# Kernel tuning notes

Measured on AMD Instinct MI355X. Metric: run time of the kernel, lower is better.

## Reference

```python
import jax, jax.numpy as jnp
from jax import lax
import numpy as np

# Dims
B_, CIN, COUT, T = 2, 64, 128, 8192
K, NM, N, DCONV, EXP = 5, 2, 16, 4, 2   # kernel, n_mamba, d_state, d_conv, expand
DI = EXP * COUT                          # d_inner = 256
DTR = (COUT + 15) // 16                  # dt_rank = 8
M = NM * 2                               # mamba instances (fwd+bwd per block)


def setup_inputs() -> dict:
    key = jax.random.key(0)
    ks = jax.random.split(key, 8)
    r = lambda k, s, sc=0.02: (jax.random.normal(k, s) * sc).astype(jnp.float32)
    return {
        "x": jax.random.normal(ks[0], (B_, CIN, T), dtype=jnp.float32),
        "conv_w": r(ks[1], (COUT, CIN, K), 0.05),
        "conv_b": jnp.zeros((COUT,), jnp.float32),
        "gn_g": jnp.ones((COUT,), jnp.float32),
        "gn_b": jnp.zeros((COUT,), jnp.float32),
        "prelu_a": jnp.full((1,), 0.25, jnp.float32),
        "ln_g": jnp.ones((NM, COUT), jnp.float32),
        "ln_b": jnp.zeros((NM, COUT), jnp.float32),
        "W_in": r(ks[2], (M, 2 * DI, COUT)),
        "conv1d_w": r(ks[3], (M, DI, 1, DCONV), 0.1),
        "conv1d_b": jnp.zeros((M, DI), jnp.float32),
        "W_xproj": r(ks[4], (M, DTR + 2 * N, DI)),
        "W_dt": r(ks[5], (M, DI, DTR), 0.1),
        "b_dt": jnp.full((M, DI), -4.0, jnp.float32),
        "A_log": jnp.broadcast_to(jnp.log(jnp.arange(1, N + 1, dtype=jnp.float32)), (M, DI, N)).copy(),
        "D_param": jnp.ones((M, DI), jnp.float32),
        "W_out": r(ks[6], (M, COUT, DI)),
    }


def _silu(x):
    return x * jax.nn.sigmoid(x)


def _layernorm(x, g, b, eps=1e-5):
    mu = x.mean(-1, keepdims=True)
    v = ((x - mu) ** 2).mean(-1, keepdims=True)
    return (x - mu) * lax.rsqrt(v + eps) * g + b


def _mamba(h, Wi, cw, cb, Wx, Wd, bd, Alog, Dp, Wo):
    # h: [B, L, d_model] -> [B, L, d_model]. Standard Mamba (S6) block.
    Bb, L, _ = h.shape
    xz = jnp.einsum('bld,ed->ble', h, Wi)               # [B,L,2*DI]
    xp, z = jnp.split(xz, 2, axis=-1)
    xc = jnp.transpose(xp, (0, 2, 1))                   # [B,DI,L]
    xc = lax.conv_general_dilated(xc, cw, (1,), [(DCONV - 1, 0)],
                                  feature_group_count=DI,
                                  dimension_numbers=('NCH', 'OIH', 'NCH')) + cb[None, :, None]
    u = _silu(jnp.transpose(xc, (0, 2, 1)))             # [B,L,DI]
    xdbl = jnp.einsum('bld,ed->ble', u, Wx)             # [B,L,DTR+2N]
    dt, Bm, Cm = jnp.split(xdbl, [DTR, DTR + N], axis=-1)
    delta = jax.nn.softplus(jnp.einsum('blr,dr->bld', dt, Wd) + bd)  # [B,L,DI]
    A = -jnp.exp(Alog)                                  # [DI,N]
    dA = jnp.exp(delta[..., None] * A)                  # [B,L,DI,N]
    dBu = (delta * u)[..., None] * Bm[:, :, None, :]    # [B,L,DI,N]

    def step(hc, inp):
        a, b, c = inp
        hc = a * hc + b                                  # [B,DI,N]
        return hc, jnp.einsum('bdn,bn->bd', hc, c)

    h0 = jnp.zeros((Bb, DI, N), dtype=h.dtype)
    _, ys = lax.scan(step, h0, (jnp.moveaxis(dA, 1, 0), jnp.moveaxis(dBu, 1, 0), jnp.moveaxis(Cm, 1, 0)))
    y = jnp.moveaxis(ys, 0, 1) + u * Dp                 # [B,L,DI]
    y = y * _silu(z)
    return jnp.einsum('ble,de->bld', y, Wo)


def reference(x, conv_w, conv_b, gn_g, gn_b, prelu_a, ln_g, ln_b, W_in,
              conv1d_w, conv1d_b, W_xproj, W_dt, b_dt, A_log, D_param, W_out):
    # Conv1d stride 2, padding K//2: [B,CIN,T] -> [B,COUT,T//2]
    h = lax.conv_general_dilated(x, conv_w, (2,), [(K // 2, K // 2)],
                                 dimension_numbers=('NCH', 'OIH', 'NCH')) + conv_b[None, :, None]
    # GroupNorm(1, COUT): normalize jointly over (C, T)
    mu = h.mean((1, 2), keepdims=True)
    v = ((h - mu) ** 2).mean((1, 2), keepdims=True)
    h = (h - mu) * lax.rsqrt(v + 1e-5) * gn_g[None, :, None] + gn_b[None, :, None]
    h = jnp.where(h >= 0, h, prelu_a[0] * h)            # PReLU (shared scalar)
    h = jnp.transpose(h, (0, 2, 1))                     # [B, L, C]
    for i in range(NM):
        hn = _layernorm(h, ln_g[i], ln_b[i])
        f, bw = 2 * i, 2 * i + 1
        yf = _mamba(hn, W_in[f], conv1d_w[f], conv1d_b[f], W_xproj[f], W_dt[f], b_dt[f], A_log[f], D_param[f], W_out[f])
        hb = jnp.flip(hn, axis=1)
        yb = jnp.flip(_mamba(hb, W_in[bw], conv1d_w[bw], conv1d_b[bw], W_xproj[bw], W_dt[bw], b_dt[bw], A_log[bw], D_param[bw], W_out[bw]), axis=1)
        h = h + yf + yb                                  # bidirectional residual
    return jnp.transpose(h, (0, 2, 1))                   # [B, COUT, T//2]
```

## Files before the change

### kernel.cpp

```cpp
#include <hip/hip_runtime.h>
#include <hip/hip_bf16.h>
#include <math.h>

constexpr int B2   = 2;
constexpr int CIN  = 64;
constexpr int COUT = 128;
constexpr int T    = 8192;
constexpr int L    = 4096;
constexpr int DI   = 256;
constexpr int NST  = 16;
constexpr int DTR  = 8;
constexpr int Q    = 32;
constexpr int NC   = 128;
constexpr int TOK  = B2 * L;

typedef __attribute__((ext_vector_type(8))) short bf16x8s;
typedef __attribute__((ext_vector_type(4))) float f32x4;

__device__ __forceinline__ float sigmoidf_(float x) { return 1.f / (1.f + __expf(-x)); }
__device__ __forceinline__ unsigned short f2bf(float f) {
    unsigned int u = __float_as_uint(f);
    unsigned int r = (u + 0x7FFFu + ((u >> 16) & 1u)) >> 16;
    return (unsigned short)r;
}
__device__ __forceinline__ float bf2f(unsigned short s) {
    return __uint_as_float((unsigned int)s << 16);
}

__global__ __launch_bounds__(256) void prep_all_kernel(
    const float* __restrict__ W_in, const float* __restrict__ W_out,
    const float* __restrict__ cw,
    unsigned short* __restrict__ Winb, unsigned short* __restrict__ Woutb,
    unsigned short* __restrict__ Wrb, float* __restrict__ stats) {
    int idx = blockIdx.x * 256 + threadIdx.x;
    if (blockIdx.x == 0 && threadIdx.x < 4) stats[threadIdx.x] = 0.f;
    if (idx < 262144) {
        Winb[idx] = f2bf(W_in[idx]);
    } else if (idx < 393216) {
        int i = idx - 262144; Woutb[i] = f2bf(W_out[i]);
    } else if (idx < 434176) {
        int i = idx - 393216;
        int co = i / 320, r = i % 320;
        int kp = r >> 6, ci = r & 63;
        Wrb[i] = f2bf(cw[co * 320 + ci * 5 + kp]);
    }
}

__global__ __launch_bounds__(256) void xpose_kernel(
    const float* __restrict__ x, unsigned short* __restrict__ xTb) {
    __shared__ float tile[64][65];
    int b = blockIdx.y, tb = blockIdx.x * 64, tid = threadIdx.x;
    #pragma unroll
    for (int i = 0; i < 16; ++i) {
        int idx = i * 256 + tid; int ci = idx >> 6, tt = idx & 63;
        tile[ci][tt] = x[((size_t)b * CIN + ci) * T + tb + tt];
    }
    __syncthreads();
    #pragma unroll
    for (int i = 0; i < 16; ++i) {
        int idx = i * 256 + tid; int tt = idx >> 6, ci = idx & 63;
        xTb[((size_t)b * T + tb + tt) * 64 + ci] = f2bf(tile[ci][tt]);
    }
}

__global__ __launch_bounds__(256) void conv_mfma_kernel(
    const unsigned short* __restrict__ xTb, const unsigned short* __restrict__ Wrb,
    const float* __restrict__ cb, float* __restrict__ h, float* __restrict__ stats) {
    const int tid = threadIdx.x;
    const int w = tid >> 6, lane = tid & 63, q = lane >> 4, c = lane & 15;
    const int t0g = blockIdx.x * 64;
    const int t0  = t0g + w * 16;
    const int ct0 = blockIdx.y * 64;
    const int b   = t0g >> 12;
    const int l   = (t0 + c) & (L - 1);
    f32x4 acc[4] = {};
    for (int kc = 0; kc < 320; kc += 32) {
        int kp  = kc >> 6;
        int ci0 = (kc & 63) + q * 8;
        int p = 2 * l + kp - 2;
        bf16x8s a = {};
        if (p >= 0 && p < T)
            a = *(const bf16x8s*)&xTb[((size_t)b * T + p) * 64 + ci0];
        #pragma unroll
        for (int i = 0; i < 4; ++i) {
            bf16x8s bb = *(const bf16x8s*)&Wrb[(size_t)(ct0 + i * 16 + c) * 320 + kc + q * 8];
            acc[i] = __builtin_amdgcn_mfma_f32_16x16x32_bf16(a, bb, acc[i], 0, 0, 0);
        }
    }
    float s = 0.f, ss = 0.f;
    #pragma unroll
    for (int i = 0; i < 4; ++i) {
        int cout = ct0 + i * 16 + c;
        float bias = cb[cout];
        #pragma unroll
        for (int r = 0; r < 4; ++r) {
            int tok = t0 + q * 4 + r;
            float v = acc[i][r] + bias;
            h[(size_t)tok * COUT + cout] = v;
            s += v; ss += v * v;
        }
    }
    #pragma unroll
    for (int off = 32; off; off >>= 1) {
        s  += __shfl_down(s,  off, 64);
        ss += __shfl_down(ss, off, 64);
    }
    if (lane == 0) {
        atomicAdd(&stats[b * 2 + 0], s);
        atomicAdd(&stats[b * 2 + 1], ss);
    }
}

__global__ __launch_bounds__(256) void gn_ln_kernel(
    float* __restrict__ h, const float* __restrict__ gn_g,
    const float* __restrict__ gn_b, const float* __restrict__ prelu_a,
    const float* __restrict__ stats, unsigned short* __restrict__ hnb,
    const float* __restrict__ lng, const float* __restrict__ lnb) {
    int wave = threadIdx.x >> 6, lane = threadIdx.x & 63;
    int t = blockIdx.x * 4 + wave;
    int b = t >> 12;
    const float n = (float)(L * COUT);
    float mu   = stats[b * 2 + 0] / n;
    float var  = stats[b * 2 + 1] / n - mu * mu;
    float rstd = rsqrtf(var + 1e-5f);
    float a = prelu_a[0];
    float* row = h + (size_t)t * COUT;
    float2 v  = *(const float2*)&row[lane * 2];
    float2 g  = *(const float2*)&gn_g[lane * 2];
    float2 bb = *(const float2*)&gn_b[lane * 2];
    v.x = (v.x - mu) * rstd * g.x + bb.x; v.x = v.x >= 0.f ? v.x : a * v.x;
    v.y = (v.y - mu) * rstd * g.y + bb.y; v.y = v.y >= 0.f ? v.y : a * v.y;
    *(float2*)&row[lane * 2] = v;
    float s = v.x + v.y, ss = v.x * v.x + v.y * v.y;
    #pragma unroll
    for (int off = 32; off; off >>= 1) {
        s  += __shfl_xor(s,  off, 64);
        ss += __shfl_xor(ss, off, 64);
    }
    float mu2 = s * (1.f / 128.f);
    float var2 = ss * (1.f / 128.f) - mu2 * mu2;
    float rstd2 = rsqrtf(var2 + 1e-5f);
    float2 gg = *(const float2*)&lng[lane * 2];
    float2 lb = *(const float2*)&lnb[lane * 2];
    ushort2 o;
    o.x = f2bf((v.x - mu2) * rstd2 * gg.x + lb.x);
    o.y = f2bf((v.y - mu2) * rstd2 * gg.y + lb.y);
    *(ushort2*)&hnb[(size_t)t * COUT + lane * 2] = o;
}

__global__ __launch_bounds__(256) void ln_kernel(
    const float* __restrict__ h, unsigned short* __restrict__ hnb,
    const float* __restrict__ g, const float* __restrict__ bta) {
    int wave = threadIdx.x >> 6, lane = threadIdx.x & 63;
    int t = blockIdx.x * 4 + wave;
    const float* row = h + (size_t)t * COUT;
    float2 v = *(const float2*)&row[lane * 2];
    float s = v.x + v.y, ss = v.x * v.x + v.y * v.y;
    #pragma unroll
    for (int off = 32; off; off >>= 1) {
        s  += __shfl_xor(s,  off, 64);
        ss += __shfl_xor(ss, off, 64);
    }
    float mu = s * (1.f / 128.f);
    float var = ss * (1.f / 128.f) - mu * mu;
    float rstd = rsqrtf(var + 1e-5f);
    float2 gg = *(const float2*)&g[lane * 2];
    float2 bb = *(const float2*)&bta[lane * 2];
    ushort2 o;
    o.x = f2bf((v.x - mu) * rstd * gg.x + bb.x);
    o.y = f2bf((v.y - mu) * rstd * gg.y + bb.y);
    *(ushort2*)&hnb[(size_t)t * COUT + lane * 2] = o;
}

__global__ __launch_bounds__(256) void inproj_dw_kernel(
    const unsigned short* __restrict__ hnb, const unsigned short* __restrict__ Winb,
    const float* __restrict__ cw, const float* __restrict__ cbias,
    float* __restrict__ u0, float* __restrict__ u1,
    unsigned short* __restrict__ zb0, unsigned short* __restrict__ zb1, int layer) {
    __shared__ float xs[80 * 68];
    const int tid = threadIdx.x;
    const int w = tid >> 6, lane = tid & 63, q = lane >> 4, c = lane & 15;
    const int tBase = blockIdx.x * 64;
    const int nBase = blockIdx.y * 64;
    const int inst = nBase >> 9;
    const int e0 = nBase & 511;
    const int m = layer * 2 + inst;
    const unsigned short* Wb = Winb + (size_t)m * 512 * 128;

    if (e0 >= 256) {
        const int t0 = tBase + w * 16;
        f32x4 acc[4] = {};
        for (int kc = 0; kc < 128; kc += 32) {
            bf16x8s a = *(const bf16x8s*)&hnb[(size_t)(t0 + c) * 128 + kc + q * 8];
            #pragma unroll
            for (int i = 0; i < 4; ++i) {
                bf16x8s bb = *(const bf16x8s*)&Wb[(size_t)(e0 + i * 16 + c) * 128 + kc + q * 8];
                acc[i] = __builtin_amdgcn_mfma_f32_16x16x32_bf16(a, bb, acc[i], 0, 0, 0);
            }
        }
        unsigned short* zb = inst ? zb1 : zb0;
        #pragma unroll
        for (int i = 0; i < 4; ++i) {
            int eo = (e0 + i * 16 + c) & 255;
            #pragma unroll
            for (int r = 0; r < 4; ++r) {
                int tok = t0 + q * 4 + r;
                float v = acc[i][r];
                zb[(size_t)tok * DI + eo] = f2bf(v * sigmoidf_(v));
            }
        }
        return;
    }
    const int winT0 = (inst == 0) ? (tBase - 16) : tBase;
    for (int pass = 0; pass < 2; ++pass) {
        if (pass == 1 && w != 0) break;
        int slot = (pass == 0) ? (w + (inst == 0 ? 1 : 0))
                               : ((inst == 0) ? 0 : 4);
        int tokA = winT0 + slot * 16 + c;
        tokA = tokA < 0 ? 0 : (tokA > TOK - 1 ? TOK - 1 : tokA);
        f32x4 acc[4] = {};
        for (int kc = 0; kc < 128; kc += 32) {
            bf16x8s a = *(const bf16x8s*)&hnb[(size_t)tokA * 128 + kc + q * 8];
            #pragma unroll
            for (int i = 0; i < 4; ++i) {
                bf16x8s bb = *(const bf16x8s*)&Wb[(size_t)(e0 + i * 16 + c) * 128 + kc + q * 8];
                acc[i] = __builtin_amdgcn_mfma_f32_16x16x32_bf16(a, bb, acc[i], 0, 0, 0);
            }
        }
        #pragma unroll
        for (int i = 0; i < 4; ++i)
            #pragma unroll
            for (int r = 0; r < 4; ++r)
                xs[(slot * 16 + q * 4 + r) * 68 + i * 16 + c] = acc[i][r];
    }
    __syncthreads();
    const int l0base = tBase & (L - 1);
    const int ch4 = tid & 15;
    const int d0 = e0 + ch4 * 4;
    float4 w0 = *(const float4*)&cw[(size_t)(m * DI + d0 + 0) * 4];
    float4 w1 = *(const float4*)&cw[(size_t)(m * DI + d0 + 1) * 4];
    float4 w2 = *(const float4*)&cw[(size_t)(m * DI + d0 + 2) * 4];
    float4 w3 = *(const float4*)&cw[(size_t)(m * DI + d0 + 3) * 4];
    float4 bias4 = *(const float4*)&cbias[m * DI + d0];
    float* ud = inst ? u1 : u0;
    #pragma unroll
    for (int p = 0; p < 4; ++p) {
        int j = p * 16 + (tid >> 4);
        float4 acc = bias4;
        #pragma unroll
        for (int k = 0; k < 4; ++k) {
            bool valid = (inst == 0) ? (l0base + j - 3 + k >= 0)
                                     : (l0base + j + 3 - k < L);
            if (valid) {
                int wj = (inst == 0) ? (j + 13 + k) : (j + 3 - k);
                float4 v = *(const float4*)&xs[wj * 68 + ch4 * 4];
                float wk0 = ((const float*)&w0)[k], wk1 = ((const float*)&w1)[k];
                float wk2 = ((const float*)&w2)[k], wk3 = ((const float*)&w3)[k];
                acc.x = fmaf(wk0, v.x, acc.x); acc.y = fmaf(wk1, v.y, acc.y);
                acc.z = fmaf(wk2, v.z, acc.z); acc.w = fmaf(wk3, v.w, acc.w);
            }
        }
        acc.x *= sigmoidf_(acc.x); acc.y *= sigmoidf_(acc.y);
        acc.z *= sigmoidf_(acc.z); acc.w *= sigmoidf_(acc.w);
        *(float4*)&ud[(size_t)(tBase + j) * DI + d0] = acc;
    }
}

__global__ __launch_bounds__(256) void xproj_kernel(
    const float* __restrict__ u0, const float* __restrict__ u1,
    const float* __restrict__ Wx, const float* __restrict__ Wdt,
    const float* __restrict__ bdt,
    float* __restrict__ dl0, float* __restrict__ dl1,
    float* __restrict__ Bm0, float* __restrict__ Bm1,
    float* __restrict__ Cm0, float* __restrict__ Cm1, int layer) {
    __shared__ float Ws[40 * 132];
    __shared__ float As[128 * 33];
    __shared__ float xd[32 * 9];
    const int tid   = threadIdx.x;
    const int tBase = blockIdx.x * 32;
    const int inst  = blockIdx.y;
    const int m     = layer * 2 + inst;
    const float* u  = inst ? u1 : u0;
    const float* Wm = Wx + (size_t)m * 40 * 256;
    const int t  = tid & 31;
    const int eq = tid >> 5;
    float acc[5] = {};
    for (int kc = 0; kc < 256; kc += 128) {
        __syncthreads();
        #pragma unroll
        for (int i = 0; i < 5; ++i) {
            int idx = i * 256 + tid;
            int e = idx >> 5, kq = idx & 31;
            float4 w4 = *(const float4*)&Wm[(size_t)e * 256 + kc + kq * 4];
            float* dstw = &Ws[e * 132 + kq * 4];
            dstw[0] = w4.x; dstw[1] = w4.y; dstw[2] = w4.z; dstw[3] = w4.w;
        }
        #pragma unroll
        for (int i = 0; i < 4; ++i) {
            int flat = i * 256 + tid;
            int tt = flat >> 5, kq = flat & 31;
            float4 v = *(const float4*)&u[(size_t)(tBase + tt) * DI + kc + kq * 4];
            As[(kq * 4 + 0) * 33 + tt] = v.x;
            As[(kq * 4 + 1) * 33 + tt] = v.y;
            As[(kq * 4 + 2) * 33 + tt] = v.z;
            As[(kq * 4 + 3) * 33 + tt] = v.w;
        }
        __syncthreads();
        #pragma unroll 4
        for (int kk = 0; kk < 128; ++kk) {
            float a = As[kk * 33 + t];
            acc[0] = fmaf(a, Ws[(eq     ) * 132 + kk], acc[0]);
            acc[1] = fmaf(a, Ws[(eq +  8) * 132 + kk], acc[1]);
            acc[2] = fmaf(a, Ws[(eq + 16) * 132 + kk], acc[2]);
            acc[3] = fmaf(a, Ws[(eq + 24) * 132 + kk], acc[3]);
            acc[4] = fmaf(a, Ws[(eq + 32) * 132 + kk], acc[4]);
        }
    }
    {
        int tok = tBase + t;
        float* Bm = inst ? Bm1 : Bm0;
        float* Cm = inst ? Cm1 : Cm0;
        xd[t * 9 + eq] = acc[0];
        Bm[(size_t)tok * NST + eq]     = acc[1];
        Bm[(size_t)tok * NST + 8 + eq] = acc[2];
        Cm[(size_t)tok * NST + eq]     = acc[3];
        Cm[(size_t)tok * NST + 8 + eq] = acc[4];
    }
    __syncthreads();
    {
        int d = tid;
        float wr[8];
        #pragma unroll
        for (int r = 0; r < 8; ++r) wr[r] = Wdt[((size_t)m * DI + d) * DTR + r];
        float bb = bdt[m * DI + d];
        float* dl = inst ? dl1 : dl0;
        #pragma unroll 4
        for (int tt = 0; tt < 32; ++tt) {
            float a2 = bb;
            #pragma unroll
            for (int r = 0; r < 8; ++r) a2 = fmaf(xd[tt * 9 + r], wr[r], a2);
            float sp = fmaxf(a2, 0.f) + __logf(1.f + __expf(-fabsf(a2)));
            dl[(size_t)(tBase + tt) * DI + d] = sp;
        }
    }
}

__global__ __launch_bounds__(256) void scan1_kernel(
    const float* __restrict__ dl0, const float* __restrict__ dl1,
    const float* __restrict__ u0,  const float* __restrict__ u1,
    const float* __restrict__ Bm0, const float* __restrict__ Bm1,
    const float* __restrict__ A_log,
    float* __restrict__ hend, float* __restrict__ dsumb, int layer) {
    const int tid = threadIdx.x;
    const int nq = tid & 3, dlane = tid >> 2;
    const int chunk = blockIdx.x & (NC - 1), dtile = blockIdx.x >> 7;
    const int b = blockIdx.y, inst = blockIdx.z;
    const int m = layer * 2 + inst, dir = inst;
    const int d = dtile * 64 + dlane;
    const float* dl = inst ? dl1 : dl0;
    const float* u  = inst ? u1  : u0;
    const float* Bm = inst ? Bm1 : Bm0;
    float4 av = *(const float4*)&A_log[((size_t)m * DI + d) * NST + nq * 4];
    const float a0 = -expf(av.x), a1 = -expf(av.y), a2 = -expf(av.z), a3 = -expf(av.w);
    const int s0 = chunk * Q;
    const int l0 = dir ? (L - 1 - s0) : s0;
    const int stp = dir ? -1 : 1;
    long iDU = ((long)(b * L + l0)) * DI + d;
    int  iB  = ((b * L + l0) << 4) + nq * 4;
    const long sDU = (long)stp * DI;
    const int  sB  = stp * NST;
    float h0 = 0.f, h1 = 0.f, h2 = 0.f, h3 = 0.f, dsum = 0.f;
    #pragma unroll 4
    for (int t = 0; t < Q; ++t) {
        float dlt = dl[iDU], uu = u[iDU];
        float4 bm = *(const float4*)&Bm[iB];
        float du = dlt * uu;
        h0 = fmaf(__expf(dlt * a0), h0, du * bm.x);
        h1 = fmaf(__expf(dlt * a1), h1, du * bm.y);
        h2 = fmaf(__expf(dlt * a2), h2, du * bm.z);
        h3 = fmaf(__expf(dlt * a3), h3, du * bm.w);
        dsum += dlt;
        iDU += sDU; iB += sB;
    }
    size_t oh = (((size_t)(inst * 2 + b) * DI + d) * NC + chunk) * NST + nq * 4;
    *(float4*)&hend[oh] = make_float4(h0, h1, h2, h3);
    if (nq == 0) dsumb[((size_t)(inst * 2 + b) * NC + chunk) * DI + d] = dsum;
}

__global__ __launch_bounds__(256) void combine_kernel(
    float* __restrict__ hend, const float* __restrict__ dsumb,
    const float* __restrict__ A_log, int layer) {
    int flat = blockIdx.x * 256 + threadIdx.x;
    int n = flat & 15;
    int d = (flat >> 4) & 255;
    int b = (flat >> 12) & 1;
    int inst = flat >> 13;
    int m = layer * 2 + inst;
    float a = -expf(A_log[((size_t)m * DI + d) * NST + n]);
    size_t baseE = (((size_t)(inst * 2 + b) * DI + d) * NC) * NST + n;
    size_t baseD = ((size_t)(inst * 2 + b) * NC) * DI + d;
    float hc = 0.f;
    #pragma unroll 4
    for (int c = 0; c < NC; ++c) {
        float tmp = hend[baseE + (size_t)c * NST];
        hend[baseE + (size_t)c * NST] = hc;
        float ds = dsumb[baseD + (size_t)c * DI];
        hc = fmaf(__expf(a * ds), hc, tmp);
    }
}

__global__ __launch_bounds__(256) void scan2_kernel(
    const float* __restrict__ dl0, const float* __restrict__ dl1,
    const float* __restrict__ u0,  const float* __restrict__ u1,
    const float* __restrict__ Bm0, const float* __restrict__ Bm1,
    const float* __restrict__ Cm0, const float* __restrict__ Cm1,
    unsigned short* __restrict__ zb0, unsigned short* __restrict__ zb1,
    const float* __restrict__ hin, const float* __restrict__ A_log,
    const float* __restrict__ Dp, int layer) {
    const int tid = threadIdx.x;
    const int nq = tid & 3, dlane = tid >> 2;
    const int chunk = blockIdx.x & (NC - 1), dtile = blockIdx.x >> 7;
    const int b = blockIdx.y, inst = blockIdx.z;
    const int m = layer * 2 + inst, dir = inst;
    const int d = dtile * 64 + dlane;
    const float* dl = inst ? dl1 : dl0;
    const float* u  = inst ? u1  : u0;
    const float* Bm = inst ? Bm1 : Bm0;
    const float* Cm = inst ? Cm1 : Cm0;
    unsigned short* zs = inst ? zb1 : zb0;
    float4 av = *(const float4*)&A_log[((size_t)m * DI + d) * NST + nq * 4];
    const float a0 = -expf(av.x), a1 = -expf(av.y), a2 = -expf(av.z), a3 = -expf(av.w);
    const float dpar = Dp[m * DI + d];
    const int s0 = chunk * Q;
    const int l0 = dir ? (L - 1 - s0) : s0;
    const int stp = dir ? -1 : 1;
    long iDU = ((long)(b * L + l0)) * DI + d;
    int  iB  = ((b * L + l0) << 4) + nq * 4;
    const long sDU = (long)stp * DI;
    const int  sB  = stp * NST;
    float4 hv = *(const float4*)&hin[(((size_t)(inst * 2 + b) * DI + d) * NC + chunk) * NST + nq * 4];
    float h0 = hv.x, h1 = hv.y, h2 = hv.z, h3 = hv.w;
    #pragma unroll 4
    for (int t = 0; t < Q; ++t) {
        float dlt = dl[iDU], uu = u[iDU];
        float4 bm = *(const float4*)&Bm[iB];
        float4 cm = *(const float4*)&Cm[iB];
        float du = dlt * uu;
        h0 = fmaf(__expf(dlt * a0), h0, du * bm.x);
        h1 = fmaf(__expf(dlt * a1), h1, du * bm.y);
        h2 = fmaf(__expf(dlt * a2), h2, du * bm.z);
        h3 = fmaf(__expf(dlt * a3), h3, du * bm.w);
        float yp = h0 * cm.x + h1 * cm.y + h2 * cm.z + h3 * cm.w;
        yp += __shfl_xor(yp, 1, 4);
        yp += __shfl_xor(yp, 2, 4);
        if (nq == 0) {
            float zv = bf2f(zs[iDU]);
            zs[iDU] = f2bf(fmaf(uu, dpar, yp) * zv);
        }
        iDU += sDU; iB += sB;
    }
}

__global__ __launch_bounds__(256) void outproj_mfma_kernel(
    const unsigned short* __restrict__ ygb0, const unsigned short* __restrict__ ygb1,
    const unsigned short* __restrict__ Woutb, float* __restrict__ h, int layer) {
    const int tid = threadIdx.x;
    const int w = tid >> 6, lane = tid & 63, q = lane >> 4, c = lane & 15;
    const int t0 = blockIdx.x * 64 + w * 16;
    const int ct0 = blockIdx.y * 32;
    f32x4 acc[2] = {};
    #pragma unroll
    for (int inst = 0; inst < 2; ++inst) {
        const unsigned short* yg = inst ? ygb1 : ygb0;
        const unsigned short* Wb = Woutb + (size_t)(layer * 2 + inst) * COUT * DI;
        for (int kc = 0; kc < 256; kc += 32) {
            bf16x8s a = *(const bf16x8s*)&yg[(size_t)(t0 + c) * DI + kc + q * 8];
            #pragma unroll
            for (int i = 0; i < 2; ++i) {
                bf16x8s bb = *(const bf16x8s*)&Wb[(size_t)(ct0 + i * 16 + c) * DI + kc + q * 8];
                acc[i] = __builtin_amdgcn_mfma_f32_16x16x32_bf16(a, bb, acc[i], 0, 0, 0);
            }
        }
    }
    #pragma unroll
    for (int i = 0; i < 2; ++i) {
        int cout = ct0 + i * 16 + c;
        #pragma unroll
        for (int r = 0; r < 4; ++r) {
            int tok = t0 + q * 4 + r;
            h[(size_t)tok * COUT + cout] += acc[i][r];
        }
    }
}

__global__ __launch_bounds__(256) void transpose_kernel(
    const float* __restrict__ h, float* __restrict__ out) {
    __shared__ float tile[32][33];
    int lt0 = blockIdx.x * 32, ct0 = blockIdx.y * 32, b = blockIdx.z;
    int c = threadIdx.x & 31, r = threadIdx.x >> 5;
    #pragma unroll
    for (int j = 0; j < 4; ++j) {
        int ll = r + 8 * j;
        tile[ll][c] = h[((size_t)b * L + lt0 + ll) * COUT + ct0 + c];
    }
    __syncthreads();
    #pragma unroll
    for (int j = 0; j < 4; ++j) {
        int cc = r + 8 * j;
        out[((size_t)b * COUT + ct0 + cc) * L + lt0 + c] = tile[c][cc];
    }
}

extern "C" void kernel_launch(void* const* d_in, const int* in_sizes, int n_in,
                              void* d_out, int out_size, void* d_ws, size_t ws_size,
                              hipStream_t stream) {
    const float* x        = (const float*)d_in[0];
    const float* conv_w   = (const float*)d_in[1];
    const float* conv_b   = (const float*)d_in[2];
    const float* gn_g     = (const float*)d_in[3];
    const float* gn_b     = (const float*)d_in[4];
    const float* prelu_a  = (const float*)d_in[5];
    const float* ln_g     = (const float*)d_in[6];
    const float* ln_b     = (const float*)d_in[7];
    const float* W_in     = (const float*)d_in[8];
    const float* conv1d_w = (const float*)d_in[9];
    const float* conv1d_b = (const float*)d_in[10];
    const float* W_xproj  = (const float*)d_in[11];
    const float* W_dt     = (const float*)d_in[12];
    const float* b_dt     = (const float*)d_in[13];
    const float* A_log    = (const float*)d_in[14];
    const float* D_param  = (const float*)d_in[15];
    const float* W_out    = (const float*)d_in[16];

    float* ws = (float*)d_ws;
    float* h     = ws;
    unsigned short* zb0 = (unsigned short*)(ws + 5242880);
    unsigned short* zb1 = (unsigned short*)(ws + 6291456);
    float* u0    = ws + 7340032;
    float* u1    = ws + 9437184;
    float* dl0   = ws + 11534336;
    float* dl1   = ws + 13631488;
    float* Bm0   = ws + 15728640;
    float* Bm1   = ws + 15859712;
    float* Cm0   = ws + 15990784;
    float* Cm1   = ws + 16121856;
    float* hend  = ws + 16252928;
    float* dsumb = ws + 18350080;
    unsigned short* Winb  = (unsigned short*)(ws + 18481152);
    unsigned short* Wrb   = (unsigned short*)(ws + 18612224);
    unsigned short* Woutb = (unsigned short*)(ws + 18632704);
    float* stats = ws + 18698240;
    unsigned short* hnb = (unsigned short*)hend;
    unsigned short* xTb = zb0;

    prep_all_kernel<<<1696, 256, 0, stream>>>(W_in, W_out, conv_w, Winb, Woutb, Wrb, stats);
    xpose_kernel<<<dim3(T / 64, B2), 256, 0, stream>>>(x, xTb);
    conv_mfma_kernel<<<dim3(TOK / 64, COUT / 64), 256, 0, stream>>>(xTb, Wrb, conv_b, h, stats);
    gn_ln_kernel<<<TOK / 4, 256, 0, stream>>>(h, gn_g, gn_b, prelu_a, stats, hnb, ln_g, ln_b);

    for (int layer = 0; layer < 2; ++layer) {
        if (layer == 1)
            ln_kernel<<<TOK / 4, 256, 0, stream>>>(h, hnb, ln_g + COUT, ln_b + COUT);
        inproj_dw_kernel<<<dim3(TOK / 64, 16), 256, 0, stream>>>(hnb, Winb, conv1d_w, conv1d_b,
                                                                 u0, u1, zb0, zb1, layer);
        xproj_kernel<<<dim3(TOK / 32, 2), 256, 0, stream>>>(u0, u1, W_xproj, W_dt, b_dt,
                                                            dl0, dl1, Bm0, Bm1, Cm0, Cm1, layer);
        scan1_kernel<<<dim3(NC * 4, B2, 2), 256, 0, stream>>>(dl0, dl1, u0, u1, Bm0, Bm1,
                                                              A_log, hend, dsumb, layer);
        combine_kernel<<<64, 256, 0, stream>>>(hend, dsumb, A_log, layer);
        scan2_kernel<<<dim3(NC * 4, B2, 2), 256, 0, stream>>>(dl0, dl1, u0, u1, Bm0, Bm1, Cm0, Cm1,
                                                              zb0, zb1, hend, A_log, D_param, layer);
        outproj_mfma_kernel<<<dim3(TOK / 64, 4), 256, 0, stream>>>(zb0, zb1, Woutb, h, layer);
    }
    transpose_kernel<<<dim3(L / 32, COUT / 32, B2), 256, 0, stream>>>(h, (float*)d_out);
}
```

Baseline: 378.6 us.

## Compute local scan outputs in pass one and apply carry correction in pass two

The first chunked scan pass now also produces the chunk-local output y (bf16) and the running cumulative delta per token. The second pass no longer re-runs the recurrence. It adds a linear correction from the incoming carried state, decayed by exp(A*cumdelta) and contracted with C, then applies the z gate. This removes the duplicated recurrence and the delta/u/B reads from pass two. In exchange, pass one writes extra y and cumulative-delta buffers, pass two reads them back, and y is rounded to bf16 before the correction is added.

```diff
diff --git a/kernel.cpp b/kernel.cpp
--- a/kernel.cpp
+++ b/kernel.cpp
@@ -349,8 +349,11 @@
     const float* __restrict__ dl0, const float* __restrict__ dl1,
     const float* __restrict__ u0,  const float* __restrict__ u1,
     const float* __restrict__ Bm0, const float* __restrict__ Bm1,
-    const float* __restrict__ A_log,
-    float* __restrict__ hend, float* __restrict__ dsumb, int layer) {
+    const float* __restrict__ Cm0, const float* __restrict__ Cm1,
+    const float* __restrict__ A_log, const float* __restrict__ Dp,
+    float* __restrict__ hend, float* __restrict__ dsumb,
+    unsigned short* __restrict__ yl0, unsigned short* __restrict__ yl1,
+    float* __restrict__ cum0, float* __restrict__ cum1, int layer) {
     const int tid = threadIdx.x;
     const int nq = tid & 3, dlane = tid >> 2;
     const int chunk = blockIdx.x & (NC - 1), dtile = blockIdx.x >> 7;
@@ -360,8 +363,12 @@
     const float* dl = inst ? dl1 : dl0;
     const float* u  = inst ? u1  : u0;
     const float* Bm = inst ? Bm1 : Bm0;
+    const float* Cm = inst ? Cm1 : Cm0;
+    unsigned short* yl = inst ? yl1 : yl0;
+    float* cum = inst ? cum1 : cum0;
     float4 av = *(const float4*)&A_log[((size_t)m * DI + d) * NST + nq * 4];
     const float a0 = -expf(av.x), a1 = -expf(av.y), a2 = -expf(av.z), a3 = -expf(av.w);
+    const float dpar = Dp[m * DI + d];
     const int s0 = chunk * Q;
     const int l0 = dir ? (L - 1 - s0) : s0;
     const int stp = dir ? -1 : 1;
@@ -374,12 +381,20 @@
     for (int t = 0; t < Q; ++t) {
         float dlt = dl[iDU], uu = u[iDU];
         float4 bm = *(const float4*)&Bm[iB];
+        float4 cm = *(const float4*)&Cm[iB];
         float du = dlt * uu;
         h0 = fmaf(__expf(dlt * a0), h0, du * bm.x);
         h1 = fmaf(__expf(dlt * a1), h1, du * bm.y);
         h2 = fmaf(__expf(dlt * a2), h2, du * bm.z);
         h3 = fmaf(__expf(dlt * a3), h3, du * bm.w);
         dsum += dlt;
+        float yp = h0 * cm.x + h1 * cm.y + h2 * cm.z + h3 * cm.w;
+        yp += __shfl_xor(yp, 1, 4);
+        yp += __shfl_xor(yp, 2, 4);
+        if (nq == 0) {
+            yl[iDU] = f2bf(fmaf(uu, dpar, yp));
+            cum[iDU] = dsum;
+        }
         iDU += sDU; iB += sB;
     }
     size_t oh = (((size_t)(inst * 2 + b) * DI + d) * NC + chunk) * NST + nq * 4;
@@ -410,27 +425,23 @@
 }
 
 __global__ __launch_bounds__(256) void scan2_kernel(
-    const float* __restrict__ dl0, const float* __restrict__ dl1,
-    const float* __restrict__ u0,  const float* __restrict__ u1,
-    const float* __restrict__ Bm0, const float* __restrict__ Bm1,
+    const float* __restrict__ cum0, const float* __restrict__ cum1,
     const float* __restrict__ Cm0, const float* __restrict__ Cm1,
+    const unsigned short* __restrict__ yl0, const unsigned short* __restrict__ yl1,
     unsigned short* __restrict__ zb0, unsigned short* __restrict__ zb1,
-    const float* __restrict__ hin, const float* __restrict__ A_log,
-    const float* __restrict__ Dp, int layer) {
+    const float* __restrict__ hin, const float* __restrict__ A_log, int layer) {
     const int tid = threadIdx.x;
     const int nq = tid & 3, dlane = tid >> 2;
     const int chunk = blockIdx.x & (NC - 1), dtile = blockIdx.x >> 7;
     const int b = blockIdx.y, inst = blockIdx.z;
     const int m = layer * 2 + inst, dir = inst;
     const int d = dtile * 64 + dlane;
-    const float* dl = inst ? dl1 : dl0;
-    const float* u  = inst ? u1  : u0;
-    const float* Bm = inst ? Bm1 : Bm0;
+    const float* cum = inst ? cum1 : cum0;
     const float* Cm = inst ? Cm1 : Cm0;
+    const unsigned short* yl = inst ? yl1 : yl0;
     unsigned short* zs = inst ? zb1 : zb0;
     float4 av = *(const float4*)&A_log[((size_t)m * DI + d) * NST + nq * 4];
     const float a0 = -expf(av.x), a1 = -expf(av.y), a2 = -expf(av.z), a3 = -expf(av.w);
-    const float dpar = Dp[m * DI + d];
     const int s0 = chunk * Q;
     const int l0 = dir ? (L - 1 - s0) : s0;
     const int stp = dir ? -1 : 1;
@@ -438,24 +449,21 @@
     int  iB  = ((b * L + l0) << 4) + nq * 4;
     const long sDU = (long)stp * DI;
     const int  sB  = stp * NST;
-    float4 hv = *(const float4*)&hin[(((size_t)(inst * 2 + b) * DI + d) * NC + chunk) * NST + nq * 4];
-    float h0 = hv.x, h1 = hv.y, h2 = hv.z, h3 = hv.w;
+    float4 pf = *(const float4*)&hin[(((size_t)(inst * 2 + b) * DI + d) * NC + chunk) * NST + nq * 4];
     #pragma unroll 4
     for (int t = 0; t < Q; ++t) {
-        float dlt = dl[iDU], uu = u[iDU];
-        float4 bm = *(const float4*)&Bm[iB];
+        float cv = cum[iDU];
         float4 cm = *(const float4*)&Cm[iB];
-        float du = dlt * uu;
-        h0 = fmaf(__expf(dlt * a0), h0, du * bm.x);
-        h1 = fmaf(__expf(dlt * a1), h1, du * bm.y);
-        h2 = fmaf(__expf(dlt * a2), h2, du * bm.z);
-        h3 = fmaf(__expf(dlt * a3), h3, du * bm.w);
-        float yp = h0 * cm.x + h1 * cm.y + h2 * cm.z + h3 * cm.w;
-        yp += __shfl_xor(yp, 1, 4);
-        yp += __shfl_xor(yp, 2, 4);
+        float corr = pf.x * cm.x * __expf(a0 * cv)
+                   + pf.y * cm.y * __expf(a1 * cv)
+                   + pf.z * cm.z * __expf(a2 * cv)
+                   + pf.w * cm.w * __expf(a3 * cv);
+        corr += __shfl_xor(corr, 1, 4);
+        corr += __shfl_xor(corr, 2, 4);
         if (nq == 0) {
+            float yv = bf2f(yl[iDU]) + corr;
             float zv = bf2f(zs[iDU]);
-            zs[iDU] = f2bf(fmaf(uu, dpar, yp) * zv);
+            zs[iDU] = f2bf(yv * zv);
         }
         iDU += sDU; iB += sB;
     }
@@ -534,6 +542,8 @@
 
     float* ws = (float*)d_ws;
     float* h     = ws;
+    float* cum0  = ws + 1048576;
+    float* cum1  = ws + 3145728;
     unsigned short* zb0 = (unsigned short*)(ws + 5242880);
     unsigned short* zb1 = (unsigned short*)(ws + 6291456);
     float* u0    = ws + 7340032;
@@ -549,7 +559,9 @@
     unsigned short* Winb  = (unsigned short*)(ws + 18481152);
     unsigned short* Wrb   = (unsigned short*)(ws + 18612224);
     unsigned short* Woutb = (unsigned short*)(ws + 18632704);
-    float* stats = ws + 18698240;
+    unsigned short* yl0   = (unsigned short*)(ws + 18698240);
+    unsigned short* yl1   = (unsigned short*)(ws + 19222528);
+    float* stats = ws + 19746816;
     unsigned short* hnb = (unsigned short*)hend;
     unsigned short* xTb = zb0;
 
@@ -565,11 +577,12 @@
                                                                  u0, u1, zb0, zb1, layer);
         xproj_kernel<<<dim3(TOK / 32, 2), 256, 0, stream>>>(u0, u1, W_xproj, W_dt, b_dt,
                                                             dl0, dl1, Bm0, Bm1, Cm0, Cm1, layer);
-        scan1_kernel<<<dim3(NC * 4, B2, 2), 256, 0, stream>>>(dl0, dl1, u0, u1, Bm0, Bm1,
-                                                              A_log, hend, dsumb, layer);
+        scan1_kernel<<<dim3(NC * 4, B2, 2), 256, 0, stream>>>(dl0, dl1, u0, u1, Bm0, Bm1, Cm0, Cm1,
+                                                              A_log, D_param, hend, dsumb,
+                                                              yl0, yl1, cum0, cum1, layer);
         combine_kernel<<<64, 256, 0, stream>>>(hend, dsumb, A_log, layer);
-        scan2_kernel<<<dim3(NC * 4, B2, 2), 256, 0, stream>>>(dl0, dl1, u0, u1, Bm0, Bm1, Cm0, Cm1,
-                                                              zb0, zb1, hend, A_log, D_param, layer);
+        scan2_kernel<<<dim3(NC * 4, B2, 2), 256, 0, stream>>>(cum0, cum1, Cm0, Cm1, yl0, yl1,
+                                                              zb0, zb1, hend, A_log, layer);
         outproj_mfma_kernel<<<dim3(TOK / 64, 4), 256, 0, stream>>>(zb0, zb1, Woutb, h, layer);
     }
     transpose_kernel<<<dim3(L / 32, COUT / 32, B2), 256, 0, stream>>>(h, (float*)d_out);
```

Measured after the change: 399.8 us. 1.06x slower.
